# Performance work log

Measured on AMD Instinct MI355X. Metric: run time of the kernel, lower is better.

## Reference

```python
import math
import jax, jax.numpy as jnp
import numpy as np

B, T, S, D, H, L, DFF, IN, PERIOD = 16, 600, 600, 1024, 8, 8, 4096, 52, 25
HD = D // H
NEG = -1e9


def _param(key, name, shape, scale=0.02):
    k = jax.random.fold_in(key, hash(name) % (2**31))
    return jax.random.normal(k, shape, dtype=jnp.float32) * scale


def setup_inputs() -> dict:
    key = jax.random.key(0)
    k1, k2, k3 = jax.random.split(key, 3)
    inp = {}
    inp["x"] = jax.random.normal(k1, (B, T, IN), dtype=jnp.float32)
    inp["memory"] = jax.random.normal(k2, (B, S, D), dtype=jnp.float32)
    inp["timesteps"] = jax.random.randint(k3, (B,), 0, 1000, dtype=jnp.int32)

    # Periodic positional encoding buffer: sinusoidal over one period, tiled.
    pos = jnp.arange(PERIOD, dtype=jnp.float32)[:, None]
    div = jnp.exp(jnp.arange(0, D, 2, dtype=jnp.float32) * (-math.log(10000.0) / D))
    pe_p = jnp.zeros((PERIOD, D), dtype=jnp.float32)
    pe_p = pe_p.at[:, 0::2].set(jnp.sin(pos * div)).at[:, 1::2].set(jnp.cos(pos * div))
    inp["pe"] = jnp.tile(pe_p, (T // PERIOD + 1, 1))[:T]  # [T, D]

    # ALiBi-style periodic bias (vectorized form of init_bi_biased_mask_faceformer).
    # alibi[h,i,j] = -slope_h * floor((i-j)/period) for j<=i, -slope_h*floor((j-i-1)/period) for j>i
    slopes = jnp.array([0.5 ** (h + 1) for h in range(H)], dtype=jnp.float32)
    di = jnp.arange(T)[:, None] - jnp.arange(T)[None, :]
    steps = jnp.where(di >= 0, di // PERIOD, (-di - 1) // PERIOD).astype(jnp.float32)
    inp["alibi"] = -slopes[:, None, None] * steps[None]  # [H, T, T]

    # Parameters
    inp["W_in"] = _param(key, "W_in", (D, IN))
    inp["b_in"] = jnp.zeros((D,), jnp.float32)
    inp["te_W1"] = _param(key, "te_W1", (D, D))
    inp["te_b1"] = jnp.zeros((D,), jnp.float32)
    inp["te_W2"] = _param(key, "te_W2", (D, D))
    inp["te_b2"] = jnp.zeros((D,), jnp.float32)
    for nm, shape in [
        ("sa_Wqkv", (L, 3 * D, D)), ("sa_bqkv", (L, 3 * D)),
        ("sa_Wo", (L, D, D)), ("sa_bo", (L, D)),
        ("ca_Wqkv", (L, 3 * D, D)), ("ca_bqkv", (L, 3 * D)),
        ("ca_Wo", (L, D, D)), ("ca_bo", (L, D)),
        ("ff_W1", (L, DFF, D)), ("ff_b1", (L, DFF)),
        ("ff_W2", (L, D, DFF)), ("ff_b2", (L, D)),
    ]:
        inp[nm] = _param(key, nm, shape)
    for nm in ["ln1_g", "ln2_g", "ln3_g"]:
        inp[nm] = jnp.ones((L, D), jnp.float32)
    for nm in ["ln1_b", "ln2_b", "ln3_b"]:
        inp[nm] = jnp.zeros((L, D), jnp.float32)
    inp["W_out"] = _param(key, "W_out", (IN, D))
    inp["b_out"] = jnp.zeros((IN,), jnp.float32)
    return inp


def _ln(x, g, b, eps=1e-5):
    mu = jnp.mean(x, axis=-1, keepdims=True)
    var = jnp.mean(jnp.square(x - mu), axis=-1, keepdims=True)
    return (x - mu) * jax.lax.rsqrt(var + eps) * g + b


def _mha(q_in, kv_in, Wqkv, bqkv, Wo, bo, bias):
    # q_in: [B,Tq,D]; kv_in: [B,Tk,D]; bias broadcastable to [B,H,Tq,Tk]
    Wq, Wk, Wv = jnp.split(Wqkv, 3, axis=0)
    bq, bk, bv = jnp.split(bqkv, 3, axis=0)
    Bn, Tq, _ = q_in.shape
    Tk = kv_in.shape[1]
    q = (q_in @ Wq.T + bq).reshape(Bn, Tq, H, HD).transpose(0, 2, 1, 3)
    k = (kv_in @ Wk.T + bk).reshape(Bn, Tk, H, HD).transpose(0, 2, 1, 3)
    v = (kv_in @ Wv.T + bv).reshape(Bn, Tk, H, HD).transpose(0, 2, 1, 3)
    scores = jnp.einsum("bhqd,bhkd->bhqk", q, k) / math.sqrt(HD) + bias
    attn = jax.nn.softmax(scores, axis=-1)
    out = jnp.einsum("bhqk,bhkd->bhqd", attn, v)
    out = out.transpose(0, 2, 1, 3).reshape(Bn, Tq, D)
    return out @ Wo.T + bo


def reference(x, memory, timesteps, pe, alibi, W_in, b_in, te_W1, te_b1, te_W2, te_b2,
              sa_Wqkv, sa_bqkv, sa_Wo, sa_bo, ca_Wqkv, ca_bqkv, ca_Wo, ca_bo,
              ff_W1, ff_b1, ff_W2, ff_b2, ln1_g, ln1_b, ln2_g, ln2_b, ln3_g, ln3_b,
              W_out, b_out):
    # --- timestep embedding (DDPM sinusoidal + 2-layer SiLU MLP) ---
    half = D // 2
    exponent = jnp.exp(-math.log(10000.0) * jnp.arange(half, dtype=jnp.float32) / (half - 1.0))
    emb = timesteps.astype(jnp.float32)[:, None] * exponent[None, :]
    t_emb = jnp.concatenate([jnp.sin(emb), jnp.cos(emb)], axis=-1)  # [B, D]
    t_emb = jax.nn.silu(t_emb @ te_W1.T + te_b1) @ te_W2.T + te_b2
    adapter = t_emb[:, None, :]  # [B, 1, D] adapter token

    # --- input projection + periodic positional encoding ---
    h = x @ W_in.T + b_in + pe[None]  # [B, T, D]

    # --- attention biases (adapter column is always attendable => zero bias) ---
    sa_bias = jnp.concatenate([jnp.zeros((H, T, 1), jnp.float32), alibi], axis=-1)[None]  # [1,H,T,1+T]
    eye = jnp.eye(T, S, dtype=jnp.float32)
    mem_bias = jnp.where(eye > 0, 0.0, NEG)  # FaceFormer diagonal-only memory mask
    mem_bias = jnp.concatenate([jnp.zeros((T, 1), jnp.float32), mem_bias], axis=-1)[None, None]  # [1,1,T,1+S]

    # --- stacked decoder layers (post-norm, adapter prepended to K/V) ---
    for l in range(L):
        x_adpt = jnp.concatenate([adapter, h], axis=1)  # [B, 1+T, D]
        h = _ln(h + _mha(h, x_adpt, sa_Wqkv[l], sa_bqkv[l], sa_Wo[l], sa_bo[l], sa_bias), ln1_g[l], ln1_b[l])
        mem_adpt = jnp.concatenate([adapter, memory], axis=1)  # [B, 1+S, D]
        h = _ln(h + _mha(h, mem_adpt, ca_Wqkv[l], ca_bqkv[l], ca_Wo[l], ca_bo[l], mem_bias), ln2_g[l], ln2_b[l])
        ff = jax.nn.relu(h @ ff_W1[l].T + ff_b1[l]) @ ff_W2[l].T + ff_b2[l]
        h = _ln(h + ff, ln3_g[l], ln3_b[l])

    return h @ W_out.T + b_out  # [B, T, IN]
```

## Files before the change

kernel.cpp:

```cpp
#include <hip/hip_runtime.h>
#include <stdint.h>

#define B_ 16
#define T_ 600
#define S_ 600
#define D_ 1024
#define H_ 8
#define HD_ 128
#define L_ 8
#define DFF_ 4096
#define IN_ 52
#define TP1 601
#define MTOK 9600
#define MPAD 9728
#define VTK 608

typedef unsigned short u16;
typedef float f32x4 __attribute__((ext_vector_type(4)));
typedef __bf16 bf16x8 __attribute__((ext_vector_type(8)));

__device__ __forceinline__ u16 f2bf(float f){
  union { float f; unsigned u; } v; v.f = f;
  v.u += 0x7FFFu + ((v.u >> 16) & 1u);
  return (u16)(v.u >> 16);
}
__device__ __forceinline__ float bf2f(u16 h){
  union { unsigned u; float f; } v; v.u = ((unsigned)h) << 16;
  return v.f;
}
__device__ __forceinline__ void gld_lds16(const void* g, void* l){
  __builtin_amdgcn_global_load_lds(
      (const __attribute__((address_space(1))) void*)(uintptr_t)g,
      (__attribute__((address_space(3))) void*)(uintptr_t)l, 16, 0, 0);
}
__device__ __forceinline__ f32x4 MM(bf16x8 a, bf16x8 b, f32x4 c){
  return __builtin_amdgcn_mfma_f32_16x16x32_bf16(a, b, c, 0, 0, 0);
}
#define BAR() asm volatile("s_barrier" ::: "memory")

template<int EPI>
__global__ __launch_bounds__(512, 2)
void k_gemm256(const u16* __restrict__ A, const u16* __restrict__ W,
               const float* __restrict__ bias, void* __restrict__ Cout,
               float* __restrict__ hres, int N, int K, int Mstore){
  __shared__ u16 lds[65536];
  const int t = threadIdx.x;
  const int w = t >> 6, l = t & 63;
  const int lr = l & 15, lg = l >> 4;
  const int wr = w >> 2, wc = w & 3;

  int lin = blockIdx.y * gridDim.x + blockIdx.x;
  const int nwg = gridDim.x * gridDim.y;
  lin = (lin & 7) * (nwg >> 3) + (lin >> 3);
  const long m0 = (long)(lin / gridDim.x) * 256;
  const long n0 = (long)(lin % gridDim.x) * 256;

  const int srow = w*8 + (l >> 3);
  const int schk = (l & 7) ^ (l >> 3);
  const u16* gA = A + (m0 + srow) * (long)K + schk * 8;
  const u16* gB = W + (n0 + srow) * (long)K + schk * 8;

  const int chk0 = ((    lg) ^ (lr & 7)) * 8;
  const int chk1 = ((4 + lg) ^ (lr & 7)) * 8;
  const int arow = (wr*128 + lr) * 64;
  const int brow = (wc*64  + lr) * 64 + 16384;

  f32x4 acc[8][4] = {};
  const int NT = K >> 6;

#define STG_A(i) gld_lds16(gA + (long)(i)*64*K + nc, (void*)(lds + nb + (i)*4096 + w*512))
#define STG_B(i) gld_lds16(gB + (long)(i)*64*K + nc, (void*)(lds + nb + 16384 + (i)*4096 + w*512))
#define LOADF(mq, CH) \
    a0 = *(const bf16x8*)(lds + bufo + arow + ((mq)*4+0)*1024 + (CH)); \
    a1 = *(const bf16x8*)(lds + bufo + arow + ((mq)*4+1)*1024 + (CH)); \
    a2 = *(const bf16x8*)(lds + bufo + arow + ((mq)*4+2)*1024 + (CH)); \
    a3 = *(const bf16x8*)(lds + bufo + arow + ((mq)*4+3)*1024 + (CH)); \
    b0 = *(const bf16x8*)(lds + bufo + brow + 0*1024 + (CH)); \
    b1 = *(const bf16x8*)(lds + bufo + brow + 1*1024 + (CH)); \
    b2 = *(const bf16x8*)(lds + bufo + brow + 2*1024 + (CH));  \
    b3 = *(const bf16x8*)(lds + bufo + brow + 3*1024 + (CH));
#define MFMA16(mq) \
    __builtin_amdgcn_s_setprio(1); \
    { const bf16x8 aa[4] = {a0,a1,a2,a3}; const bf16x8 bb4[4] = {b0,b1,b2,b3}; \
      _Pragma("unroll") for (int i_ = 0; i_ < 4; i_++) \
        _Pragma("unroll") for (int j_ = 0; j_ < 4; j_++) \
          acc[(mq)*4+i_][j_] = MM(aa[i_], bb4[j_], acc[(mq)*4+i_][j_]); } \
    __builtin_amdgcn_s_setprio(0);

  { const int nb = 0; const long nc = 0;
    STG_B(0); STG_B(1); STG_B(2); STG_B(3);
    STG_A(0); STG_A(2); STG_A(1); STG_A(3);
  }
  asm volatile("s_waitcnt vmcnt(2)" ::: "memory");
  BAR();

  int bufo = 0;
  for (int tt = 0; tt < NT; ++tt){
    const int nb = bufo ^ 32768;
    const bool st = (tt + 1 < NT);
    const long nc = (long)(tt + 1) * 64;
    bf16x8 a0,a1,a2,a3,b0,b1,b2,b3;
    LOADF(0, chk0);
    if (st){ STG_B(0); STG_B(1); }
    BAR();
    MFMA16(0);
    BAR();
    LOADF(0, chk1);
    if (st){ STG_B(2); STG_B(3); asm volatile("s_waitcnt vmcnt(4)" ::: "memory"); }
    else   {                     asm volatile("s_waitcnt vmcnt(0)" ::: "memory"); }
    BAR();
    MFMA16(0);
    BAR();
    LOADF(1, chk0);
    if (st){ STG_A(0); STG_A(2); }
    BAR();
    MFMA16(1);
    BAR();
    LOADF(1, chk1);
    if (st){ STG_A(1); STG_A(3); asm volatile("s_waitcnt vmcnt(2)" ::: "memory"); }
    BAR();
    MFMA16(1);
    BAR();
    bufo = nb;
  }
#undef STG_A
#undef STG_B
#undef LOADF
#undef MFMA16

  const int r4 = lg * 4;
#pragma unroll
  for (int nf = 0; nf < 4; nf++){
    const long col = n0 + wc*64 + nf*16 + lr;
    const float bv = bias[col];
#pragma unroll
    for (int mf = 0; mf < 8; mf++){
      const long row = m0 + wr*128 + mf*16 + r4;
      if (EPI == 2 && row >= Mstore) continue;
#pragma unroll
      for (int r = 0; r < 4; r++){
        float v = acc[mf][nf][r] + bv;
        if (EPI == 1) v = fmaxf(v, 0.f);
        if (EPI == 2) hres[(row + r) * (long)N + col] += v;
        else          ((u16*)Cout)[(row + r) * (long)N + col] = f2bf(v);
      }
    }
  }
}

template<int EPI>
__global__ __launch_bounds__(512, 2)
void k_gemm_n64(const u16* __restrict__ A, const u16* __restrict__ W,
                const float* __restrict__ bias, void* __restrict__ Cout,
                float* __restrict__ hres, int N, int K, int Mstore){
  __shared__ u16 lds[40960];
  const int t = threadIdx.x;
  const int w = t >> 6, l = t & 63;
  const int lr = l & 15, lg = l >> 4;
  const int wr2 = w >> 2, wc4 = w & 3;

  int lin = blockIdx.y * gridDim.x + blockIdx.x;
  const int nwg = gridDim.x * gridDim.y;
  lin = (lin & 7) * (nwg >> 3) + (lin >> 3);
  const long m0 = (long)(lin / gridDim.x) * 256;
  const long n0 = (long)(lin % gridDim.x) * 64;

  const int srow = w*8 + (l >> 3);
  const int schk = (l & 7) ^ (l >> 3);
  const u16* gA = A + (m0 + srow) * (long)K + schk * 8;
  const u16* gB = W + (n0 + srow) * (long)K + schk * 8;

  const int swz = lr & 7;
  const int arow_lo = wr2*8192 + lr*64;
  const int arow_hi = arow_lo + 4096;
  const int browb   = 16384 + (wc4*16 + lr)*64;

  f32x4 acc[8] = {};
  const int NT = K >> 6;

#define STG_A64(i) gld_lds16(gA + (long)(i)*64*K + nc, (void*)(lds + nb + (i)*4096 + w*512))
#define STG_B64()  gld_lds16(gB + nc,                  (void*)(lds + nb + 16384 + w*512))

  { const int nb = 0; const long nc = 0;
    STG_B64(); STG_A64(0); STG_A64(2); STG_A64(1); STG_A64(3);
  }
  asm volatile("s_waitcnt vmcnt(2)" ::: "memory");
  BAR();

  int bufo = 0;
  for (int tt = 0; tt < NT; ++tt){
    const int nb = (bufo ^ 20480);
    const bool st = (tt + 1 < NT);
    const long nc = (long)(tt + 1) * 64;
    const int c0 = (lg ^ swz) * 8;
    const int c1 = ((4 + lg) ^ swz) * 8;
    bf16x8 a00,a10,a20,a30,a01,a11,a21,a31,b0,b1;
    b0  = *(const bf16x8*)(lds + bufo + browb + c0);
    b1  = *(const bf16x8*)(lds + bufo + browb + c1);
    a00 = *(const bf16x8*)(lds + bufo + arow_lo + 0*1024 + c0);
    a10 = *(const bf16x8*)(lds + bufo + arow_lo + 1*1024 + c0);
    a20 = *(const bf16x8*)(lds + bufo + arow_lo + 2*1024 + c0);
    a30 = *(const bf16x8*)(lds + bufo + arow_lo + 3*1024 + c0);
    a01 = *(const bf16x8*)(lds + bufo + arow_lo + 0*1024 + c1);
    a11 = *(const bf16x8*)(lds + bufo + arow_lo + 1*1024 + c1);
    a21 = *(const bf16x8*)(lds + bufo + arow_lo + 2*1024 + c1);
    a31 = *(const bf16x8*)(lds + bufo + arow_lo + 3*1024 + c1);
    if (st){ STG_B64(); STG_A64(0); STG_A64(2); }
    __builtin_amdgcn_s_setprio(1);
    acc[0] = MM(a00, b0, acc[0]); acc[0] = MM(a01, b1, acc[0]);
    acc[1] = MM(a10, b0, acc[1]); acc[1] = MM(a11, b1, acc[1]);
    acc[2] = MM(a20, b0, acc[2]); acc[2] = MM(a21, b1, acc[2]);
    acc[3] = MM(a30, b0, acc[3]); acc[3] = MM(a31, b1, acc[3]);
    __builtin_amdgcn_s_setprio(0);
    if (st) asm volatile("s_waitcnt vmcnt(3)" ::: "memory");
    else    asm volatile("s_waitcnt vmcnt(0)" ::: "memory");
    BAR();
    a00 = *(const bf16x8*)(lds + bufo + arow_hi + 0*1024 + c0);
    a10 = *(const bf16x8*)(lds + bufo + arow_hi + 1*1024 + c0);
    a20 = *(const bf16x8*)(lds + bufo + arow_hi + 2*1024 + c0);
    a30 = *(const bf16x8*)(lds + bufo + arow_hi + 3*1024 + c0);
    a01 = *(const bf16x8*)(lds + bufo + arow_hi + 0*1024 + c1);
    a11 = *(const bf16x8*)(lds + bufo + arow_hi + 1*1024 + c1);
    a21 = *(const bf16x8*)(lds + bufo + arow_hi + 2*1024 + c1);
    a31 = *(const bf16x8*)(lds + bufo + arow_hi + 3*1024 + c1);
    if (st){ STG_A64(1); STG_A64(3); }
    __builtin_amdgcn_s_setprio(1);
    acc[4] = MM(a00, b0, acc[4]); acc[4] = MM(a01, b1, acc[4]);
    acc[5] = MM(a10, b0, acc[5]); acc[5] = MM(a11, b1, acc[5]);
    acc[6] = MM(a20, b0, acc[6]); acc[6] = MM(a21, b1, acc[6]);
    acc[7] = MM(a30, b0, acc[7]); acc[7] = MM(a31, b1, acc[7]);
    __builtin_amdgcn_s_setprio(0);
    if (st) asm volatile("s_waitcnt vmcnt(2)" ::: "memory");
    BAR();
    bufo = nb;
  }
#undef STG_A64
#undef STG_B64

  const int r4 = lg * 4;
  const long col = n0 + wc4*16 + lr;
  const float bv = bias[col];
#pragma unroll
  for (int mf = 0; mf < 8; mf++){
    const long row = m0 + wr2*128 + mf*16 + r4;
    if (EPI == 2 && row >= Mstore) continue;
#pragma unroll
    for (int r = 0; r < 4; r++){
      float v = acc[mf][r] + bv;
      if (EPI == 1) v = fmaxf(v, 0.f);
      if (EPI == 2) hres[(row + r) * (long)N + col] += v;
      else          ((u16*)Cout)[(row + r) * (long)N + col] = f2bf(v);
    }
  }
}

__global__ __launch_bounds__(256)
void k_gemm_in(const u16* __restrict__ A, const u16* __restrict__ W,
               const float* __restrict__ bias, const float* __restrict__ pe,
               float* __restrict__ hf, u16* __restrict__ hbf, u16* __restrict__ xad){
  __shared__ u16 sA[128*64];
  __shared__ u16 sB[128*64];
  const int t = threadIdx.x;
  const int w = t >> 6, l = t & 63;
  const int lr = l & 15, lg = l >> 4;
  const long m0 = (long)blockIdx.y * 128;
  const long n0 = (long)blockIdx.x * 128;
  const int wm = (w >> 1) << 6, wn = (w & 1) << 6;
  const int srow = t >> 3;
  const int schk = (t & 7) ^ (srow & 7);
  const u16* gA = A + (m0 + srow) * 64 + schk * 8;
  const u16* gB = W + (n0 + srow) * 64 + schk * 8;
#pragma unroll
  for (int i = 0; i < 4; i++){
    gld_lds16(gA + i*32*64, (void*)(sA + i*2048 + (t>>6)*512));
    gld_lds16(gB + i*32*64, (void*)(sB + i*2048 + (t>>6)*512));
  }
  asm volatile("s_waitcnt vmcnt(0)" ::: "memory");
  __syncthreads();
  f32x4 acc[4][4] = {};
#pragma unroll
  for (int kk = 0; kk < 2; kk++){
    bf16x8 af[4], bfv[4];
#pragma unroll
    for (int i = 0; i < 4; i++){
      const int row = wm + i*16 + lr;
      af[i] = *(const bf16x8*)(sA + row*64 + ((kk*4+lg)^(row&7))*8);
    }
#pragma unroll
    for (int j = 0; j < 4; j++){
      const int row = wn + j*16 + lr;
      bfv[j] = *(const bf16x8*)(sB + row*64 + ((kk*4+lg)^(row&7))*8);
    }
#pragma unroll
    for (int i = 0; i < 4; i++)
#pragma unroll
      for (int j = 0; j < 4; j++)
        acc[i][j] = MM(af[i], bfv[j], acc[i][j]);
  }
  const int r0 = lg * 4;
#pragma unroll
  for (int j = 0; j < 4; j++){
    const long col = n0 + wn + j*16 + lr;
    const float bv = bias[col];
#pragma unroll
    for (int i = 0; i < 4; i++){
      const long row = m0 + wm + i*16 + r0;
#pragma unroll
      for (int r = 0; r < 4; r++){
        const long rr = row + r;
        if (rr >= MTOK) continue;
        const float v = acc[i][j][r] + bv + pe[(rr % 25)*1024 + col];
        const u16 hv = f2bf(v);
        hf[rr*1024 + col] = v;
        hbf[rr*1024 + col] = hv;
        const long bq = rr / 600, tq = rr % 600;
        xad[((bq*TP1 + 1 + tq) << 10) + col] = hv;
      }
    }
  }
}

__global__ __launch_bounds__(256)
void k_gemm_out(const u16* __restrict__ A, const u16* __restrict__ W,
                const float* __restrict__ bias, float* __restrict__ outp){
  __shared__ u16 sA[128*32];
  __shared__ u16 sB[128*32];
  const int t = threadIdx.x;
  const int w = t >> 6, l = t & 63;
  const long m0 = (long)blockIdx.y * 128;
  const int wm = (w >> 1) << 6, wn = (w & 1) << 6;
  const int K = 1024;
  f32x4 acc[4][4] = {};
  const char* gA0 = (const char*)(A + (m0 + (t >> 2)) * (long)K) + (t & 3) * 16;
  const char* gA1 = gA0 + 64 * (long)K * 2;
  const char* gB0 = (const char*)(W + (long)(t >> 2) * K) + (t & 3) * 16;
  const char* gB1 = gB0 + 64 * (long)K * 2;
  char* lA = (char*)sA + w * 1024;
  char* lB = (char*)sB + w * 1024;
  const int lr = l & 15;
  const int lkb = (l >> 4) * 16;
  for (long k0 = 0; k0 < K; k0 += 32){
    const long kb = k0 * 2;
    gld_lds16(gA0 + kb, lA);
    gld_lds16(gA1 + kb, lA + 4096);
    gld_lds16(gB0 + kb, lB);
    gld_lds16(gB1 + kb, lB + 4096);
    __syncthreads();
    bf16x8 af[4], bfv[4];
#pragma unroll
    for (int i = 0; i < 4; i++)
      af[i] = *(const bf16x8*)((const char*)sA + (wm + i*16 + lr)*64 + lkb);
#pragma unroll
    for (int j = 0; j < 4; j++)
      bfv[j] = *(const bf16x8*)((const char*)sB + (wn + j*16 + lr)*64 + lkb);
#pragma unroll
    for (int i = 0; i < 4; i++)
#pragma unroll
      for (int j = 0; j < 4; j++)
        acc[i][j] = MM(af[i], bfv[j], acc[i][j]);
    __syncthreads();
  }
  const int r0 = (l >> 4) * 4;
#pragma unroll
  for (int j = 0; j < 4; j++){
    const int col = wn + j*16 + lr;
    if (col >= IN_) continue;
    const float bv = bias[col];
#pragma unroll
    for (int i = 0; i < 4; i++){
      const long row = m0 + wm + i*16 + r0;
#pragma unroll
      for (int r = 0; r < 4; r++)
        outp[(row + r) * (long)IN_ + col] = acc[i][j][r] + bv;
    }
  }
}

__global__ __launch_bounds__(256)
void k_vtrans(const u16* __restrict__ qkv, u16* __restrict__ vt){
  const int b = blockIdx.z;
  const int h = blockIdx.y >> 1;
  const int d0 = (blockIdx.y & 1) * 64;
  const int k0 = blockIdx.x * 64;
  __shared__ u16 tile[64][72];
  const int t = threadIdx.x;
#pragma unroll
  for (int it = 0; it < 2; it++){
    const int idx = t + it*256;
    const int kk = idx >> 3;
    const int dd = (idx & 7) * 8;
    const int kabs = k0 + kk;
    union { bf16x8 v; u16 us[8]; } u;
    if (kabs <= 600)
      u.v = *(const bf16x8*)(qkv + ((long)b*TP1 + kabs)*3072 + 2048 + h*128 + d0 + dd);
    else {
#pragma unroll
      for (int j = 0; j < 8; j++) u.us[j] = 0;
    }
    *(bf16x8*)(&tile[kk][dd]) = u.v;
  }
  __syncthreads();
#pragma unroll
  for (int it = 0; it < 2; it++){
    const int idx = t + it*256;
    const int dd = idx >> 3;
    const int kc = (idx & 7) * 8;
    if (k0 + kc + 7 < VTK){
      union { uint4 o; u16 us[8]; } u;
#pragma unroll
      for (int j = 0; j < 8; j++) u.us[j] = tile[kc + j][dd];
      *(uint4*)(vt + ((long)(b*8 + h)*128 + d0 + dd)*VTK + k0 + kc) = u.o;
    }
  }
}

__global__ __launch_bounds__(256)
void k_sa_attn3(const u16* __restrict__ qkv, const u16* __restrict__ vt,
                u16* __restrict__ outp){
  const int id = blockIdx.x;
  const int g  = id & 127;
  const int qt = id >> 7;
  const int b = g >> 3, h = g & 7;
  const int w = threadIdx.x >> 6, l = threadIdx.x & 63;
  const int lr = l & 15, lg = l >> 4;
  const int q0 = qt * 64 + w * 16;
  const float scale = 0.08838834764831845f;
  const float slope = exp2f(-(float)(h + 1));

  __shared__ u16 Kl[2][4096];
  __shared__ u16 Vl[2][4096];
  __shared__ u16 Pl[4][16*32];
  __shared__ float cS[4][16];
  __shared__ float iS[4][16];

  const long bb = (long)b * TP1;
  const u16* qptr = qkv + (bb + 1 + q0 + lr) * 3072 + h * 128 + lg * 8;
  bf16x8 aq[4];
#pragma unroll
  for (int kk = 0; kk < 4; kk++) aq[kk] = *(const bf16x8*)(qptr + kk * 32);

  const int kj0 = w*2, kj1 = w*2 + 1;
  const int kkey0 = kj0*4 + (l >> 4), kkey1 = kj1*4 + (l >> 4);
  const u16* kg0 = qkv + (bb + kkey0)*3072 + 1024 + h*128 + (((l&15) ^ (kkey0&7)))*8;
  const u16* kg1 = qkv + (bb + kkey1)*3072 + 1024 + h*128 + (((l&15) ^ (kkey1&7)))*8;
  const u16* vbase = vt + (long)(b*8 + h) * 128 * VTK;
  const int vd0 = kj0*16 + (l >> 2), vd1 = kj1*16 + (l >> 2);
  const u16* vg0 = vbase + (long)vd0*VTK + ((l&3) ^ (vd0&3))*8;
  const u16* vg1 = vbase + (long)vd1*VTK + ((l&3) ^ (vd1&3))*8;

#define STAGE(buf, kb) \
  gld_lds16(kg0 + (long)(kb)*3072, (void*)(Kl[buf] + kj0*512)); \
  gld_lds16(kg1 + (long)(kb)*3072, (void*)(Kl[buf] + kj1*512)); \
  gld_lds16(vg0 + (kb),            (void*)(Vl[buf] + kj0*512)); \
  gld_lds16(vg1 + (kb),            (void*)(Vl[buf] + kj1*512));

  f32x4 o[8] = {};
  float mrow[4] = {-1e30f, -1e30f, -1e30f, -1e30f};
  float lsum[4] = {0.f, 0.f, 0.f, 0.f};

  STAGE(0, 0);
  asm volatile("s_waitcnt vmcnt(0)" ::: "memory");
  BAR();

  for (int kt = 0; kt < 19; kt++){
    const int kb0 = kt * 32;
    const int cur = kt & 1;
    const bool st = (kt < 18);
    if (st){ STAGE(cur ^ 1, kb0 + 32); }
    f32x4 s0 = {}, s1 = {};
#pragma unroll
    for (int kk = 0; kk < 4; kk++){
      const int sw = ((kk*4 + lg) ^ (lr & 7)) * 8;
      bf16x8 bk0 = *(const bf16x8*)(Kl[cur] + lr*128 + sw);
      bf16x8 bk1 = *(const bf16x8*)(Kl[cur] + (lr+16)*128 + sw);
      s0 = MM(aq[kk], bk0, s0);
      s1 = MM(aq[kk], bk1, s1);
    }
#pragma unroll
    for (int r = 0; r < 4; r++){
      const int iq = q0 + lg * 4 + r;
      float v0 = s0[r] * scale, v1 = s1[r] * scale;
      const int k0a = kb0 + lr, k1a = kb0 + 16 + lr;
      if (k0a >= 601) v0 = -1e30f;
      else if (k0a > 0){
        const int j = k0a - 1, di = iq - j;
        const int st2 = di >= 0 ? di/25 : (-di-1)/25;
        v0 -= slope * (float)st2;
      }
      if (k1a >= 601) v1 = -1e30f;
      else {
        const int j = k1a - 1, di = iq - j;
        const int st2 = di >= 0 ? di/25 : (-di-1)/25;
        v1 -= slope * (float)st2;
      }
      float mx = fmaxf(v0, v1);
#pragma unroll
      for (int d = 8; d >= 1; d >>= 1) mx = fmaxf(mx, __shfl_xor(mx, d, 64));
      const float mnew = fmaxf(mrow[r], mx);
      const float corr = __expf(mrow[r] - mnew);
      const float p0 = __expf(v0 - mnew);
      const float p1 = __expf(v1 - mnew);
      float rs = p0 + p1;
#pragma unroll
      for (int d = 8; d >= 1; d >>= 1) rs += __shfl_xor(rs, d, 64);
      lsum[r] = lsum[r] * corr + rs;
      mrow[r] = mnew;
      if (lr == 0) cS[w][lg*4 + r] = corr;
      Pl[w][(lg*4 + r)*32 + lr]      = f2bf(p0);
      Pl[w][(lg*4 + r)*32 + 16 + lr] = f2bf(p1);
    }
    const float c = cS[w][lr];
    const bool resc = __any(c != 1.0f);
    const bf16x8 pa = *(const bf16x8*)(&Pl[w][lr*32 + lg*8]);
#pragma unroll
    for (int dc = 0; dc < 8; dc++){
      const int d = dc*16 + lr;
      const bf16x8 va = *(const bf16x8*)(Vl[cur] + d*32 + ((lg ^ (d & 3))*8));
      if (resc){
#pragma unroll
        for (int rr = 0; rr < 4; rr++) o[dc][rr] *= c;
      }
      o[dc] = MM(va, pa, o[dc]);
    }
    if (st){
      asm volatile("s_waitcnt vmcnt(0)" ::: "memory");
      BAR();
    }
  }
#undef STAGE
#pragma unroll
  for (int r = 0; r < 4; r++)
    if (lr == 0) iS[w][lg*4 + r] = 1.f / lsum[r];
  const int tq = q0 + lr;
  if (tq < 600){
    const float inv = iS[w][lr];
    u16* op = outp + ((long)b*600 + tq) * 1024 + h * 128;
#pragma unroll
    for (int dc = 0; dc < 8; dc++){
      union { uint2 o8; u16 us[4]; } pk;
#pragma unroll
      for (int rr = 0; rr < 4; rr++) pk.us[rr] = f2bf(o[dc][rr] * inv);
      *(uint2*)(op + dc*16 + lg*4) = pk.o8;
    }
  }
}

__global__ __launch_bounds__(256)
void k_ca_attn(const u16* __restrict__ qca, const u16* __restrict__ kv,
               u16* __restrict__ outp){
  const int wid = blockIdx.x * 4 + (threadIdx.x >> 6);
  const int l = threadIdx.x & 63;
  if (wid >= MTOK) return;
  const int b = wid / 600, t = wid % 600;
  const u16* q  = qca + (long)wid * 1024;
  const u16* ka = kv + ((long)b * TP1) * 2048;
  const u16* km = kv + ((long)(b * TP1 + 1 + t)) * 2048;
  const float scale = 0.08838834764831845f;
#pragma unroll
  for (int h = 0; h < 8; h++){
    const int d = h*128 + l*2;
    const float q0 = bf2f(q[d]),  q1 = bf2f(q[d+1]);
    float s0 = q0*bf2f(ka[d]) + q1*bf2f(ka[d+1]);
    float s1 = q0*bf2f(km[d]) + q1*bf2f(km[d+1]);
#pragma unroll
    for (int dd = 32; dd >= 1; dd >>= 1){
      s0 += __shfl_xor(s0, dd, 64);
      s1 += __shfl_xor(s1, dd, 64);
    }
    s0 *= scale; s1 *= scale;
    const float mx = fmaxf(s0, s1);
    const float e0 = __expf(s0 - mx), e1 = __expf(s1 - mx);
    const float inv = 1.f / (e0 + e1);
    const float o0 = (e0*bf2f(ka[1024+d])   + e1*bf2f(km[1024+d]))   * inv;
    const float o1 = (e0*bf2f(ka[1024+d+1]) + e1*bf2f(km[1024+d+1])) * inv;
    const unsigned pack = (unsigned)f2bf(o0) | ((unsigned)f2bf(o1) << 16);
    *(unsigned*)(outp + (long)wid*1024 + d) = pack;
  }
}

__global__ __launch_bounds__(256)
void k_ln2(float* __restrict__ hf, const float* __restrict__ g,
           const float* __restrict__ bb, u16* __restrict__ hbf,
           u16* __restrict__ xad){
  const long m = blockIdx.x;
  float* r = hf + m*1024;
  float vals[4];
  float sum = 0.f, sumsq = 0.f;
#pragma unroll
  for (int i = 0; i < 4; i++){
    const int idx = threadIdx.x + i*256;
    const float v = r[idx];
    vals[i] = v; sum += v; sumsq += v*v;
  }
#pragma unroll
  for (int d = 32; d >= 1; d >>= 1){ sum += __shfl_xor(sum,d,64); sumsq += __shfl_xor(sumsq,d,64); }
  __shared__ float red[8];
  const int w = threadIdx.x >> 6;
  if ((threadIdx.x & 63) == 0){ red[w] = sum; red[4+w] = sumsq; }
  __syncthreads();
  sum   = red[0]+red[1]+red[2]+red[3];
  sumsq = red[4]+red[5]+red[6]+red[7];
  const float mu  = sum * (1.f/1024.f);
  const float var = sumsq * (1.f/1024.f) - mu*mu;
  const float rstd = rsqrtf(var + 1e-5f);
  u16* xrow = nullptr;
  if (xad){
    const long bq = m / 600, tq = m % 600;
    xrow = xad + ((bq*TP1 + 1 + tq) << 10);
  }
#pragma unroll
  for (int i = 0; i < 4; i++){
    const int idx = threadIdx.x + i*256;
    const float y = (vals[i] - mu) * rstd * g[idx] + bb[idx];
    const u16 hv = f2bf(y);
    r[idx] = y;
    hbf[m*1024+idx] = hv;
    if (xad) xrow[idx] = hv;
  }
}

__global__ void k_temb_sin(const int* __restrict__ ts, float* __restrict__ emb){
  const int b = blockIdx.x;
  const float t = (float)ts[b];
  for (int j = threadIdx.x; j < 1024; j += 256){
    const int jj = j < 512 ? j : j - 512;
    const float ex = expf(-9.210340371976184f * (float)jj / 511.0f);
    const float v = t * ex;
    emb[b*1024 + j] = (j < 512) ? sinf(v) : cosf(v);
  }
}

__global__ void k_te_mm(const float* __restrict__ in, const float* __restrict__ W,
                        const float* __restrict__ bv, float* __restrict__ outp,
                        int act, u16* __restrict__ xad, u16* __restrict__ mad){
  __shared__ float row[1024];
  const int b = blockIdx.y;
  for (int k = threadIdx.x; k < 1024; k += 256) row[k] = in[b*1024 + k];
  __syncthreads();
  const int n = blockIdx.x*256 + threadIdx.x;
  const float* wr = W + (long)n*1024;
  float s = 0.f;
  for (int k = 0; k < 1024; k += 4){
    const float4 w4 = *(const float4*)(wr + k);
    s += row[k]*w4.x + row[k+1]*w4.y + row[k+2]*w4.z + row[k+3]*w4.w;
  }
  s += bv[n];
  if (act) s = s / (1.f + expf(-s));
  outp[b*1024 + n] = s;
  if (xad){
    const u16 h = f2bf(s);
    xad[((long)b*TP1)*1024 + n] = h;
    mad[((long)b*TP1)*1024 + n] = h;
  }
}

__global__ void k_convert_weights(const float* __restrict__ sqkv, const float* __restrict__ swo,
                                  const float* __restrict__ cqkv, const float* __restrict__ cwo,
                                  const float* __restrict__ fw1,  const float* __restrict__ fw2,
                                  u16* __restrict__ wbuf){
  const long idx = ((long)blockIdx.x*256 + threadIdx.x) * 8;
  const float* src; long off;
  if      (idx <  3145728L){ src = sqkv; off = idx; }
  else if (idx <  4194304L){ src = swo;  off = idx -  3145728L; }
  else if (idx <  7340032L){ src = cqkv; off = idx -  4194304L; }
  else if (idx <  8388608L){ src = cwo;  off = idx -  7340032L; }
  else if (idx < 12582912L){ src = fw1;  off = idx -  8388608L; }
  else                     { src = fw2;  off = idx - 12582912L; }
  const float4 a = *(const float4*)(src + off);
  const float4 c = *(const float4*)(src + off + 4);
  uint4 o;
  o.x = (unsigned)f2bf(a.x) | ((unsigned)f2bf(a.y) << 16);
  o.y = (unsigned)f2bf(a.z) | ((unsigned)f2bf(a.w) << 16);
  o.z = (unsigned)f2bf(c.x) | ((unsigned)f2bf(c.y) << 16);
  o.w = (unsigned)f2bf(c.z) | ((unsigned)f2bf(c.w) << 16);
  *(uint4*)(wbuf + idx) = o;
}

__global__ void k_convert_wout(const float* __restrict__ src, u16* __restrict__ dst){
  const int i = blockIdx.x*256 + threadIdx.x;
  const int row = i >> 10;
  dst[i] = (row < IN_) ? f2bf(src[i]) : (u16)0;
}

__global__ void k_convert_x(const float* __restrict__ x, u16* __restrict__ dst){
  const int i = blockIdx.x*256 + threadIdx.x;
  const int row = i >> 6, c = i & 63;
  float v = 0.f;
  if (row < MTOK && c < IN_) v = x[(long)row*IN_ + c];
  dst[i] = f2bf(v);
}

__global__ void k_convert_win(const float* __restrict__ wi, u16* __restrict__ dst){
  const int i = blockIdx.x*256 + threadIdx.x;
  const int row = i >> 6, c = i & 63;
  dst[i] = (c < IN_) ? f2bf(wi[(long)row*IN_ + c]) : (u16)0;
}

__global__ void k_build_memadpt(const float* __restrict__ mem, u16* __restrict__ mad){
  const long i = ((long)blockIdx.x*256 + threadIdx.x) * 8;
  const long tok = i >> 10, col = i & 1023;
  const long b = tok / 600, s = tok % 600;
  const float4 a = *(const float4*)(mem + i);
  const float4 c = *(const float4*)(mem + i + 4);
  uint4 o;
  o.x = (unsigned)f2bf(a.x) | ((unsigned)f2bf(a.y) << 16);
  o.y = (unsigned)f2bf(a.z) | ((unsigned)f2bf(a.w) << 16);
  o.z = (unsigned)f2bf(c.x) | ((unsigned)f2bf(c.y) << 16);
  o.w = (unsigned)f2bf(c.z) | ((unsigned)f2bf(c.w) << 16);
  *(uint4*)(mad + ((b*TP1 + 1 + s) << 10) + col) = o;
}

extern "C" void kernel_launch(void* const* d_in, const int* in_sizes, int n_in,
                              void* d_out, int out_size, void* d_ws, size_t ws_size,
                              hipStream_t stream){
  const float* x        = (const float*)d_in[0];
  const float* memory   = (const float*)d_in[1];
  const int*   tsteps   = (const int*)  d_in[2];
  const float* pe       = (const float*)d_in[3];
  const float* W_in     = (const float*)d_in[5];
  const float* b_in     = (const float*)d_in[6];
  const float* te_W1    = (const float*)d_in[7];
  const float* te_b1    = (const float*)d_in[8];
  const float* te_W2    = (const float*)d_in[9];
  const float* te_b2    = (const float*)d_in[10];
  const float* sa_Wqkv  = (const float*)d_in[11];
  const float* sa_bqkv  = (const float*)d_in[12];
  const float* sa_Wo    = (const float*)d_in[13];
  const float* sa_bo    = (const float*)d_in[14];
  const float* ca_Wqkv  = (const float*)d_in[15];
  const float* ca_bqkv  = (const float*)d_in[16];
  const float* ca_Wo    = (const float*)d_in[17];
  const float* ca_bo    = (const float*)d_in[18];
  const float* ff_W1    = (const float*)d_in[19];
  const float* ff_b1    = (const float*)d_in[20];
  const float* ff_W2    = (const float*)d_in[21];
  const float* ff_b2    = (const float*)d_in[22];
  const float* ln1_g    = (const float*)d_in[23];
  const float* ln2_g    = (const float*)d_in[24];
  const float* ln3_g    = (const float*)d_in[25];
  const float* ln1_b    = (const float*)d_in[26];
  const float* ln2_b    = (const float*)d_in[27];
  const float* ln3_b    = (const float*)d_in[28];
  const float* W_out    = (const float*)d_in[29];
  const float* b_out    = (const float*)d_in[30];

  char* ws = (char*)d_ws;
  float* h_f    = (float*)(ws + 0);
  u16*   h_bf   = (u16*)  (ws + 39321600);
  u16*   attn_bf= (u16*)  (ws + 58982400);
  u16*   xadpt  = (u16*)  (ws + 78643200);
  u16*   madpt  = (u16*)  (ws + 98336768);
  u16*   qkv    = (u16*)  (ws + 118030336);
  u16*   ffb    = (u16*)  (ws + 177799168);
  u16*   wbuf   = (u16*)  (ws + 257490944);
  float* temb_a = (float*)(ws + 177799168);
  float* temb_b = (float*)(ws + 177864704);
  u16*   vtg    = (u16*)  (ws + 177799168 + 262144);
  u16*   x_bf   = wbuf;
  u16*   win_bf = wbuf + 622592;
  u16*   wout_bf= wbuf;

  u16* qca  = qkv;
  u16* kvca = qkv + (long)MPAD * 1024;

  k_temb_sin<<<dim3(16), dim3(256), 0, stream>>>(tsteps, temb_a);
  k_te_mm<<<dim3(4,16), dim3(256), 0, stream>>>(temb_a, te_W1, te_b1, temb_b, 1, (u16*)nullptr, (u16*)nullptr);
  k_te_mm<<<dim3(4,16), dim3(256), 0, stream>>>(temb_b, te_W2, te_b2, temb_a, 0, xadpt, madpt);
  k_build_memadpt<<<dim3(4800), dim3(256), 0, stream>>>(memory, madpt);
  k_convert_x<<<dim3(2432), dim3(256), 0, stream>>>(x, x_bf);
  k_convert_win<<<dim3(256), dim3(256), 0, stream>>>(W_in, win_bf);
  k_gemm_in<<<dim3(8,76), dim3(256), 0, stream>>>(x_bf, win_bf, b_in, pe, h_f, h_bf, xadpt);

  for (int l = 0; l < L_; l++){
    k_convert_weights<<<dim3(8192), dim3(256), 0, stream>>>(
        sa_Wqkv + (long)l*3145728, sa_Wo + (long)l*1048576,
        ca_Wqkv + (long)l*3145728, ca_Wo + (long)l*1048576,
        ff_W1 + (long)l*4194304,  ff_W2 + (long)l*4194304, wbuf);
    k_gemm256<0><<<dim3(12,38), dim3(512), 0, stream>>>(xadpt, wbuf, sa_bqkv + l*3072, (void*)qkv, h_f, 3072, 1024, MPAD);
    k_vtrans<<<dim3(10,16,16), dim3(256), 0, stream>>>(qkv, vtg);
    k_sa_attn3<<<dim3(1280), dim3(256), 0, stream>>>(qkv, vtg, attn_bf);
    k_gemm_n64<2><<<dim3(16,38), dim3(512), 0, stream>>>(attn_bf, wbuf + 3145728, sa_bo + l*1024, nullptr, h_f, 1024, 1024, MTOK);
    k_ln2<<<dim3(9600), dim3(256), 0, stream>>>(h_f, ln1_g + l*1024, ln1_b + l*1024, h_bf, (u16*)nullptr);
    k_gemm_n64<0><<<dim3(16,38), dim3(512), 0, stream>>>(h_bf, wbuf + 4194304, ca_bqkv + l*3072, (void*)qca, h_f, 1024, 1024, MPAD);
    k_gemm_n64<0><<<dim3(32,38), dim3(512), 0, stream>>>(madpt, wbuf + 4194304 + 1048576, ca_bqkv + l*3072 + 1024, (void*)kvca, h_f, 2048, 1024, MPAD);
    k_ca_attn<<<dim3(2400), dim3(256), 0, stream>>>(qca, kvca, attn_bf);
    k_gemm_n64<2><<<dim3(16,38), dim3(512), 0, stream>>>(attn_bf, wbuf + 7340032, ca_bo + l*1024, nullptr, h_f, 1024, 1024, MTOK);
    k_ln2<<<dim3(9600), dim3(256), 0, stream>>>(h_f, ln2_g + l*1024, ln2_b + l*1024, h_bf, (u16*)nullptr);
    k_gemm256<1><<<dim3(16,38), dim3(512), 0, stream>>>(h_bf, wbuf + 8388608, ff_b1 + l*4096, (void*)ffb, h_f, 4096, 1024, MPAD);
    k_gemm_n64<2><<<dim3(16,38), dim3(512), 0, stream>>>(ffb, wbuf + 12582912, ff_b2 + l*1024, nullptr, h_f, 1024, 4096, MTOK);
    k_ln2<<<dim3(9600), dim3(256), 0, stream>>>(h_f, ln3_g + l*1024, ln3_b + l*1024, h_bf, xadpt);
  }
  k_convert_wout<<<dim3(512), dim3(256), 0, stream>>>(W_out, wout_bf);
  k_gemm_out<<<dim3(1,75), dim3(256), 0, stream>>>(h_bf, wout_bf, b_out, (float*)d_out);
}
```

Baseline: 5.863 ms.

## Restructure n64 GEMM to 4 waves with 64x64 per-wave tiles

Rewrites the 256x64-tile GEMM so it runs with 256 threads (4 waves) instead of 512, and each wave now owns a 64x64 output block computed as a 4x4 grid of MFMA tiles, in place of a 128x16 strip. This raises MFMA work per LDS fragment load (8 fragments feed 16 MFMAs) and removes the split half-step barrier. The prefetch is simplified to issue the whole next tile up front and wait with vmcnt(0) each iteration. The trade-offs are fewer waves per block for hiding latency, more accumulator registers, and coarser load/compute overlap.

```diff
diff --git a/kernel.cpp b/kernel.cpp
--- a/kernel.cpp
+++ b/kernel.cpp
@@ -149,7 +149,7 @@
 }
 
 template<int EPI>
-__global__ __launch_bounds__(512, 2)
+__global__ __launch_bounds__(256, 2)
 void k_gemm_n64(const u16* __restrict__ A, const u16* __restrict__ W,
                 const float* __restrict__ bias, void* __restrict__ Cout,
                 float* __restrict__ hres, int N, int K, int Mstore){
@@ -157,7 +157,6 @@
   const int t = threadIdx.x;
   const int w = t >> 6, l = t & 63;
   const int lr = l & 15, lg = l >> 4;
-  const int wr2 = w >> 2, wc4 = w & 3;
 
   int lin = blockIdx.y * gridDim.x + blockIdx.x;
   const int nwg = gridDim.x * gridDim.y;
@@ -171,85 +170,79 @@
   const u16* gB = W + (n0 + srow) * (long)K + schk * 8;
 
   const int swz = lr & 7;
-  const int arow_lo = wr2*8192 + lr*64;
-  const int arow_hi = arow_lo + 4096;
-  const int browb   = 16384 + (wc4*16 + lr)*64;
-
-  f32x4 acc[8] = {};
+  const int arowb = w*4096 + lr*64;
+  const int browb = 16384 + lr*64;
+
+  f32x4 acc[4][4] = {};
   const int NT = K >> 6;
 
-#define STG_A64(i) gld_lds16(gA + (long)(i)*64*K + nc, (void*)(lds + nb + (i)*4096 + w*512))
-#define STG_B64()  gld_lds16(gB + nc,                  (void*)(lds + nb + 16384 + w*512))
+#define STG_A3(i) gld_lds16(gA + (long)(i)*32*K + nc, (void*)(lds + nb + (i)*2048 + w*512))
+#define STG_B3(j) gld_lds16(gB + (long)(j)*32*K + nc, (void*)(lds + nb + 16384 + (j)*2048 + w*512))
 
   { const int nb = 0; const long nc = 0;
-    STG_B64(); STG_A64(0); STG_A64(2); STG_A64(1); STG_A64(3);
-  }
-  asm volatile("s_waitcnt vmcnt(2)" ::: "memory");
+    STG_B3(0); STG_B3(1);
+    STG_A3(0); STG_A3(1); STG_A3(2); STG_A3(3);
+    STG_A3(4); STG_A3(5); STG_A3(6); STG_A3(7);
+  }
+  asm volatile("s_waitcnt vmcnt(0)" ::: "memory");
   BAR();
 
   int bufo = 0;
   for (int tt = 0; tt < NT; ++tt){
-    const int nb = (bufo ^ 20480);
+    const int nb = bufo ^ 20480;
     const bool st = (tt + 1 < NT);
     const long nc = (long)(tt + 1) * 64;
-    const int c0 = (lg ^ swz) * 8;
-    const int c1 = ((4 + lg) ^ swz) * 8;
-    bf16x8 a00,a10,a20,a30,a01,a11,a21,a31,b0,b1;
-    b0  = *(const bf16x8*)(lds + bufo + browb + c0);
-    b1  = *(const bf16x8*)(lds + bufo + browb + c1);
-    a00 = *(const bf16x8*)(lds + bufo + arow_lo + 0*1024 + c0);
-    a10 = *(const bf16x8*)(lds + bufo + arow_lo + 1*1024 + c0);
-    a20 = *(const bf16x8*)(lds + bufo + arow_lo + 2*1024 + c0);
-    a30 = *(const bf16x8*)(lds + bufo + arow_lo + 3*1024 + c0);
-    a01 = *(const bf16x8*)(lds + bufo + arow_lo + 0*1024 + c1);
-    a11 = *(const bf16x8*)(lds + bufo + arow_lo + 1*1024 + c1);
-    a21 = *(const bf16x8*)(lds + bufo + arow_lo + 2*1024 + c1);
-    a31 = *(const bf16x8*)(lds + bufo + arow_lo + 3*1024 + c1);
-    if (st){ STG_B64(); STG_A64(0); STG_A64(2); }
-    __builtin_amdgcn_s_setprio(1);
-    acc[0] = MM(a00, b0, acc[0]); acc[0] = MM(a01, b1, acc[0]);
-    acc[1] = MM(a10, b0, acc[1]); acc[1] = MM(a11, b1, acc[1]);
-    acc[2] = MM(a20, b0, acc[2]); acc[2] = MM(a21, b1, acc[2]);
-    acc[3] = MM(a30, b0, acc[3]); acc[3] = MM(a31, b1, acc[3]);
-    __builtin_amdgcn_s_setprio(0);
-    if (st) asm volatile("s_waitcnt vmcnt(3)" ::: "memory");
-    else    asm volatile("s_waitcnt vmcnt(0)" ::: "memory");
-    BAR();
-    a00 = *(const bf16x8*)(lds + bufo + arow_hi + 0*1024 + c0);
-    a10 = *(const bf16x8*)(lds + bufo + arow_hi + 1*1024 + c0);
-    a20 = *(const bf16x8*)(lds + bufo + arow_hi + 2*1024 + c0);
-    a30 = *(const bf16x8*)(lds + bufo + arow_hi + 3*1024 + c0);
-    a01 = *(const bf16x8*)(lds + bufo + arow_hi + 0*1024 + c1);
-    a11 = *(const bf16x8*)(lds + bufo + arow_hi + 1*1024 + c1);
-    a21 = *(const bf16x8*)(lds + bufo + arow_hi + 2*1024 + c1);
-    a31 = *(const bf16x8*)(lds + bufo + arow_hi + 3*1024 + c1);
-    if (st){ STG_A64(1); STG_A64(3); }
-    __builtin_amdgcn_s_setprio(1);
-    acc[4] = MM(a00, b0, acc[4]); acc[4] = MM(a01, b1, acc[4]);
-    acc[5] = MM(a10, b0, acc[5]); acc[5] = MM(a11, b1, acc[5]);
-    acc[6] = MM(a20, b0, acc[6]); acc[6] = MM(a21, b1, acc[6]);
-    acc[7] = MM(a30, b0, acc[7]); acc[7] = MM(a31, b1, acc[7]);
-    __builtin_amdgcn_s_setprio(0);
-    if (st) asm volatile("s_waitcnt vmcnt(2)" ::: "memory");
+    if (st){
+      STG_B3(0); STG_B3(1);
+      STG_A3(0); STG_A3(1); STG_A3(2); STG_A3(3);
+      STG_A3(4); STG_A3(5); STG_A3(6); STG_A3(7);
+    }
+#pragma unroll
+    for (int kh = 0; kh < 2; kh++){
+      const int ch = ((kh*4 + lg) ^ swz) * 8;
+      bf16x8 a0,a1,a2,a3,b0,b1,b2,b3;
+      a0 = *(const bf16x8*)(lds + bufo + arowb + 0*1024 + ch);
+      a1 = *(const bf16x8*)(lds + bufo + arowb + 1*1024 + ch);
+      a2 = *(const bf16x8*)(lds + bufo + arowb + 2*1024 + ch);
+      a3 = *(const bf16x8*)(lds + bufo + arowb + 3*1024 + ch);
+      b0 = *(const bf16x8*)(lds + bufo + browb + 0*1024 + ch);
+      b1 = *(const bf16x8*)(lds + bufo + browb + 1*1024 + ch);
+      b2 = *(const bf16x8*)(lds + bufo + browb + 2*1024 + ch);
+      b3 = *(const bf16x8*)(lds + bufo + browb + 3*1024 + ch);
+      __builtin_amdgcn_s_setprio(1);
+      acc[0][0] = MM(a0,b0,acc[0][0]); acc[0][1] = MM(a0,b1,acc[0][1]);
+      acc[0][2] = MM(a0,b2,acc[0][2]); acc[0][3] = MM(a0,b3,acc[0][3]);
+      acc[1][0] = MM(a1,b0,acc[1][0]); acc[1][1] = MM(a1,b1,acc[1][1]);
+      acc[1][2] = MM(a1,b2,acc[1][2]); acc[1][3] = MM(a1,b3,acc[1][3]);
+      acc[2][0] = MM(a2,b0,acc[2][0]); acc[2][1] = MM(a2,b1,acc[2][1]);
+      acc[2][2] = MM(a2,b2,acc[2][2]); acc[2][3] = MM(a2,b3,acc[2][3]);
+      acc[3][0] = MM(a3,b0,acc[3][0]); acc[3][1] = MM(a3,b1,acc[3][1]);
+      acc[3][2] = MM(a3,b2,acc[3][2]); acc[3][3] = MM(a3,b3,acc[3][3]);
+      __builtin_amdgcn_s_setprio(0);
+    }
+    if (st) asm volatile("s_waitcnt vmcnt(0)" ::: "memory");
     BAR();
     bufo = nb;
   }
-#undef STG_A64
-#undef STG_B64
+#undef STG_A3
+#undef STG_B3
 
   const int r4 = lg * 4;
-  const long col = n0 + wc4*16 + lr;
-  const float bv = bias[col];
-#pragma unroll
-  for (int mf = 0; mf < 8; mf++){
-    const long row = m0 + wr2*128 + mf*16 + r4;
-    if (EPI == 2 && row >= Mstore) continue;
-#pragma unroll
-    for (int r = 0; r < 4; r++){
-      float v = acc[mf][r] + bv;
-      if (EPI == 1) v = fmaxf(v, 0.f);
-      if (EPI == 2) hres[(row + r) * (long)N + col] += v;
-      else          ((u16*)Cout)[(row + r) * (long)N + col] = f2bf(v);
+#pragma unroll
+  for (int nf = 0; nf < 4; nf++){
+    const long col = n0 + nf*16 + lr;
+    const float bv = bias[col];
+#pragma unroll
+    for (int mf = 0; mf < 4; mf++){
+      const long row = m0 + w*64 + mf*16 + r4;
+      if (EPI == 2 && row >= Mstore) continue;
+#pragma unroll
+      for (int r = 0; r < 4; r++){
+        float v = acc[mf][nf][r] + bv;
+        if (EPI == 1) v = fmaxf(v, 0.f);
+        if (EPI == 2) hres[(row + r) * (long)N + col] += v;
+        else          ((u16*)Cout)[(row + r) * (long)N + col] = f2bf(v);
+      }
     }
   }
 }
@@ -779,15 +772,15 @@
     k_gemm256<0><<<dim3(12,38), dim3(512), 0, stream>>>(xadpt, wbuf, sa_bqkv + l*3072, (void*)qkv, h_f, 3072, 1024, MPAD);
     k_vtrans<<<dim3(10,16,16), dim3(256), 0, stream>>>(qkv, vtg);
     k_sa_attn3<<<dim3(1280), dim3(256), 0, stream>>>(qkv, vtg, attn_bf);
-    k_gemm_n64<2><<<dim3(16,38), dim3(512), 0, stream>>>(attn_bf, wbuf + 3145728, sa_bo + l*1024, nullptr, h_f, 1024, 1024, MTOK);
+    k_gemm_n64<2><<<dim3(16,38), dim3(256), 0, stream>>>(attn_bf, wbuf + 3145728, sa_bo + l*1024, nullptr, h_f, 1024, 1024, MTOK);
     k_ln2<<<dim3(9600), dim3(256), 0, stream>>>(h_f, ln1_g + l*1024, ln1_b + l*1024, h_bf, (u16*)nullptr);
-    k_gemm_n64<0><<<dim3(16,38), dim3(512), 0, stream>>>(h_bf, wbuf + 4194304, ca_bqkv + l*3072, (void*)qca, h_f, 1024, 1024, MPAD);
-    k_gemm_n64<0><<<dim3(32,38), dim3(512), 0, stream>>>(madpt, wbuf + 4194304 + 1048576, ca_bqkv + l*3072 + 1024, (void*)kvca, h_f, 2048, 1024, MPAD);
+    k_gemm_n64<0><<<dim3(16,38), dim3(256), 0, stream>>>(h_bf, wbuf + 4194304, ca_bqkv + l*3072, (void*)qca, h_f, 1024, 1024, MPAD);
+    k_gemm_n64<0><<<dim3(32,38), dim3(256), 0, stream>>>(madpt, wbuf + 4194304 + 1048576, ca_bqkv + l*3072 + 1024, (void*)kvca, h_f, 2048, 1024, MPAD);
     k_ca_attn<<<dim3(2400), dim3(256), 0, stream>>>(qca, kvca, attn_bf);
-    k_gemm_n64<2><<<dim3(16,38), dim3(512), 0, stream>>>(attn_bf, wbuf + 7340032, ca_bo + l*1024, nullptr, h_f, 1024, 1024, MTOK);
+    k_gemm_n64<2><<<dim3(16,38), dim3(256), 0, stream>>>(attn_bf, wbuf + 7340032, ca_bo + l*1024, nullptr, h_f, 1024, 1024, MTOK);
     k_ln2<<<dim3(9600), dim3(256), 0, stream>>>(h_f, ln2_g + l*1024, ln2_b + l*1024, h_bf, (u16*)nullptr);
     k_gemm256<1><<<dim3(16,38), dim3(512), 0, stream>>>(h_bf, wbuf + 8388608, ff_b1 + l*4096, (void*)ffb, h_f, 4096, 1024, MPAD);
-    k_gemm_n64<2><<<dim3(16,38), dim3(512), 0, stream>>>(ffb, wbuf + 12582912, ff_b2 + l*1024, nullptr, h_f, 1024, 4096, MTOK);
+    k_gemm_n64<2><<<dim3(16,38), dim3(256), 0, stream>>>(ffb, wbuf + 12582912, ff_b2 + l*1024, nullptr, h_f, 1024, 4096, MTOK);
     k_ln2<<<dim3(9600), dim3(256), 0, stream>>>(h_f, ln3_g + l*1024, ln3_b + l*1024, h_bf, xadpt);
   }
   k_convert_wout<<<dim3(512), dim3(256), 0, stream>>>(W_out, wout_bf);
```

After: 6.223 ms. +6.1%, slower.
